# Optimization experiments

Hardware: AMD Instinct MI355X
Metric: run time of the kernel (lower is better)

## Reference

```python
import jax, jax.numpy as jnp
import numpy as np

NR = 5000            # number of sampled center points
H, W = 480, 640      # depth map resolution
P = NR * (NR - 1) // 2  # number of ordered pairs (i < j) = 12,497,500


def setup_inputs() -> dict:
    key = jax.random.key(0)
    k1, k2, k3, k4 = jax.random.split(key, 4)
    x = jax.random.normal(k1, (H, W), dtype=jnp.float32)
    rows = jax.random.randint(k2, (NR,), 0, H)
    cols = jax.random.randint(k3, (NR,), 0, W)
    centers = jnp.stack([rows, cols], axis=1).astype(jnp.int32)  # [NR, 2]
    # relative-depth ground truth labels in {-1, 0, +1}; mask = |gt|
    gt = jax.random.randint(k4, (P,), -1, 2).astype(jnp.float32)
    return {"x": x, "gt": gt, "centers": centers}


def reference(x, gt, centers):
    # gather predicted depths at the NR sampled pixel locations
    z = x[centers[:, 0], centers[:, 1]]            # [NR]
    # all pairs i<j in the same row-major order as the original double loop
    ii, jj = jnp.triu_indices(NR, k=1)             # each [P]
    d = z[ii] - z[jj]                              # z_A - z_B, [P]
    mask = jnp.abs(gt)                             # [P]
    # logistic ranking loss where gt != 0, squared loss where gt == 0
    loss = mask * jnp.log1p(jnp.exp(-gt * d)) + (1.0 - mask) * d * d
    return jnp.sum(loss) / jnp.float32(P)
```

## Files before the change

kernel.cpp:

```cpp
#include <hip/hip_runtime.h>
#include <stdint.h>

#define NR 5000
#define NRM1 4999
#define W 640
#define NBLK 2500
#define NG 5
#define PCOUNT 12497500.0f
#define LOG2E 1.44269504088896340736f
#define LN2   0.69314718055994530942f

typedef float float4u __attribute__((ext_vector_type(4)));
struct __attribute__((packed, aligned(4))) f4wrap { float4u v; };

__device__ __forceinline__ float4u load4u(const float* p) {
    return ((const f4wrap*)p)->v;
}

__global__ void gather_z(const float* __restrict__ x,
                         const int* __restrict__ centers,
                         float* __restrict__ z) {
    int t = blockIdx.x * blockDim.x + threadIdx.x;
    if (t < NR) {
        const int2 rc = ((const int2*)centers)[t];
        z[t] = x[rc.x * W + rc.y];
    }
}

__global__ __launch_bounds__(256) void pair_loss(const float* __restrict__ gt,
                                                 const float* __restrict__ z,
                                                 float* __restrict__ partials) {
    __shared__ float sz[NR];
    __shared__ float wsum[4];
    const int tid = threadIdx.x;
    const int b = blockIdx.x;

    const float4* __restrict__ zf4 = (const float4*)z;
    for (int t = tid; t < NR / 4; t += 256)
        *(float4*)&sz[4 * t] = zf4[t];
    __syncthreads();

    const int r1 = b, r2 = NR - 2 - b;
    const int len1 = NRM1 - r1;
    const int off1 = r1 * NRM1 - (r1 * (r1 - 1)) / 2;
    const int off2 = r2 * NRM1 - (r2 * (r2 - 1)) / 2;
    const int off2v = off2 - len1;
    const int vmax = (r2 > r1) ? 5000 : len1;
    const float zr1 = sz[r1], zr2 = sz[r2];

    float4u g4[NG];
    int cb[NG];
    #pragma unroll
    for (int k = 0; k < NG; ++k) {
        const int vb = 4 * tid + 1024 * k;
        const int c = min(vb, vmax - 4);
        cb[k] = c;
        const float* base = (c < len1) ? (gt + off1) : (gt + off2v);
        g4[k] = load4u(base + c);
    }
    #pragma unroll
    for (int k = 0; k < NG; ++k) {
        const int c = cb[k];
        if (c < len1 && c + 3 >= len1) {
            #pragma unroll
            for (int e = 0; e < 4; ++e)
                if (c + e >= len1) g4[k][e] = gt[off2v + c + e];
        }
    }

    float a0 = 0.0f, a1 = 0.0f, a2 = 0.0f, a3 = 0.0f;
    #pragma unroll
    for (int k = 0; k < NG; ++k) {
        const int c = cb[k];
        float l[4];
        #pragma unroll
        for (int e = 0; e < 4; ++e) {
            const int ce = c + e;
            const bool in1 = ce < len1;
            const float zj = sz[ce + (in1 ? r1 + 1 : 0)];
            const float zr = in1 ? zr1 : zr2;
            const float g = g4[k][e];
            const float s  = zj - zr;
            const float sl = s * LOG2E;
            const float lg = __log2f(1.0f + exp2f(g * sl));
            l[e] = (g != 0.0f) ? lg : s * sl;
        }
        const float gs = (l[0] + l[1]) + (l[2] + l[3]);
        const float gv = (4 * tid + 1024 * k < vmax) ? gs : 0.0f;
        if      ((k & 3) == 0) a0 += gv;
        else if ((k & 3) == 1) a1 += gv;
        else if ((k & 3) == 2) a2 += gv;
        else                   a3 += gv;
    }
    float acc = (a0 + a1) + (a2 + a3);

    for (int o = 32; o > 0; o >>= 1) acc += __shfl_down(acc, o, 64);
    if ((tid & 63) == 0) wsum[tid >> 6] = acc;
    __syncthreads();
    if (tid == 0)
        partials[b] = (wsum[0] + wsum[1]) + (wsum[2] + wsum[3]);
}

__global__ __launch_bounds__(256) void final_reduce(const float* __restrict__ partials,
                                                    float* __restrict__ out) {
    __shared__ float wsum[4];
    float acc = 0.0f;
    const float4* __restrict__ p4 = (const float4*)partials;
    for (int t = threadIdx.x; t < NBLK / 4; t += 256) {
        const float4 v = p4[t];
        acc += (v.x + v.y) + (v.z + v.w);
    }
    for (int o = 32; o > 0; o >>= 1) acc += __shfl_down(acc, o, 64);
    if ((threadIdx.x & 63) == 0) wsum[threadIdx.x >> 6] = acc;
    __syncthreads();
    if (threadIdx.x == 0)
        out[0] = ((wsum[0] + wsum[1]) + (wsum[2] + wsum[3])) * (LN2 / PCOUNT);
}

extern "C" void kernel_launch(void* const* d_in, const int* in_sizes, int n_in,
                              void* d_out, int out_size, void* d_ws, size_t ws_size,
                              hipStream_t stream) {
    const float* x       = (const float*)d_in[0];
    const float* gt      = (const float*)d_in[1];
    const int*   centers = (const int*)d_in[2];
    float* out = (float*)d_out;

    float* z        = (float*)d_ws;
    float* partials = z + NR;

    gather_z<<<(NR + 255) / 256, 256, 0, stream>>>(x, centers, z);
    pair_loss<<<NBLK, 256, 0, stream>>>(gt, z, partials);
    final_reduce<<<1, 256, 0, stream>>>(partials, out);
}
```

Before: 25.22 us.

## Compute pairwise loss in packed fp16 with pre-scaled, shifted half2 z arrays

Stores the gathered depths as pre-scaled (by log2e) fp16 pairs in two arrays offset by one element, so each thread can read eight z values with one aligned 16-byte load regardless of row parity. This removes the shared-memory staging and its barrier. The loss is evaluated branch-free with packed half2 math: softplus via exp2/log2, plus a squared term weighted by (1-g^2). Each thread handles 8 pairs per group instead of 4, and partial sums are accumulated in half2. fp16 accumulation and transcendental evaluation cut ALU work but risk significant precision loss, and adding ~5000 terms per block in half may overflow the tolerance.

```diff
diff --git a/kernel.cpp b/kernel.cpp
--- a/kernel.cpp
+++ b/kernel.cpp
@@ -1,98 +1,132 @@
 #include <hip/hip_runtime.h>
+#include <hip/hip_fp16.h>
 #include <stdint.h>
 
 #define NR 5000
 #define NRM1 4999
 #define W 640
 #define NBLK 2500
-#define NG 5
+#define PTOT 12497500
 #define PCOUNT 12497500.0f
 #define LOG2E 1.44269504088896340736f
 #define LN2   0.69314718055994530942f
+#define NH2   2512
 
 typedef float float4u __attribute__((ext_vector_type(4)));
 struct __attribute__((packed, aligned(4))) f4wrap { float4u v; };
-
 __device__ __forceinline__ float4u load4u(const float* p) {
     return ((const f4wrap*)p)->v;
+}
+__device__ __forceinline__ __half2 f2h2(float f) {
+    union { float f; __half2 h; } u; u.f = f; return u.h;
 }
 
 __global__ void gather_z(const float* __restrict__ x,
                          const int* __restrict__ centers,
-                         float* __restrict__ z) {
-    int t = blockIdx.x * blockDim.x + threadIdx.x;
-    if (t < NR) {
-        const int2 rc = ((const int2*)centers)[t];
-        z[t] = x[rc.x * W + rc.y];
+                         __half2* __restrict__ zsA,
+                         __half2* __restrict__ zsB) {
+    const int i = blockIdx.x * blockDim.x + threadIdx.x;
+    if (i >= NH2) return;
+    float v[3];
+    #pragma unroll
+    for (int e = 0; e < 3; ++e) {
+        const int t = 2 * i + e;
+        if (t < NR) {
+            const int2 rc = ((const int2*)centers)[t];
+            v[e] = x[rc.x * W + rc.y] * LOG2E;
+        } else {
+            v[e] = 0.0f;
+        }
     }
+    zsA[i] = __floats2half2_rn(v[0], v[1]);
+    zsB[i] = __floats2half2_rn(v[1], v[2]);
 }
 
 __global__ __launch_bounds__(256) void pair_loss(const float* __restrict__ gt,
-                                                 const float* __restrict__ z,
+                                                 const __half2* __restrict__ zsA,
+                                                 const __half2* __restrict__ zsB,
                                                  float* __restrict__ partials) {
-    __shared__ float sz[NR];
     __shared__ float wsum[4];
     const int tid = threadIdx.x;
     const int b = blockIdx.x;
 
-    const float4* __restrict__ zf4 = (const float4*)z;
-    for (int t = tid; t < NR / 4; t += 256)
-        *(float4*)&sz[4 * t] = zf4[t];
-    __syncthreads();
-
     const int r1 = b, r2 = NR - 2 - b;
-    const int len1 = NRM1 - r1;
+    const int len1 = NRM1 - b;
+    const int len1p = (len1 + 7) & ~7;
+    const int len2 = (r2 > r1) ? (b + 1) : 0;
+    const int vmaxp = len1p + len2;
     const int off1 = r1 * NRM1 - (r1 * (r1 - 1)) / 2;
     const int off2 = r2 * NRM1 - (r2 * (r2 - 1)) / 2;
-    const int off2v = off2 - len1;
-    const int vmax = (r2 > r1) ? 5000 : len1;
-    const float zr1 = sz[r1], zr2 = sz[r2];
+    const int off2p = off2 - len1p;
+    const int j1 = r1 + 1;
+    const int j2 = r2 + 1 - len1p;
+    const __half2* __restrict__ pz1 = (j1 & 1) ? zsB : zsA;
+    const __half2* __restrict__ pz2 = (j2 & 1) ? zsB : zsA;
+    const int h1 = j1 >> 1;
+    const int h2o = j2 >> 1;
+    const int G = (vmaxp - 1) & ~7;
 
-    float4u g4[NG];
-    int cb[NG];
-    #pragma unroll
-    for (int k = 0; k < NG; ++k) {
-        const int vb = 4 * tid + 1024 * k;
-        const int c = min(vb, vmax - 4);
-        cb[k] = c;
-        const float* base = (c < len1) ? (gt + off1) : (gt + off2v);
-        g4[k] = load4u(base + c);
-    }
-    #pragma unroll
-    for (int k = 0; k < NG; ++k) {
-        const int c = cb[k];
-        if (c < len1 && c + 3 >= len1) {
-            #pragma unroll
-            for (int e = 0; e < 4; ++e)
-                if (c + e >= len1) g4[k][e] = gt[off2v + c + e];
+    const __half* __restrict__ zflat = (const __half*)zsA;
+    const __half2 zr1h = __half2half2(zflat[r1]);
+    const __half2 zr2h = __half2half2(zflat[r2]);
+    const __half2 one2 = __float2half2_rn(1.0f);
+    const __half2 ln2h = __float2half2_rn(LN2);
+    const __half2 neg1 = __float2half2_rn(-1.0f);
+
+    __half2 acc01 = __float2half2_rn(0.0f);
+    __half2 acc23 = __float2half2_rn(0.0f);
+    float accS = 0.0f;
+
+    auto doGroup = [&](int vb) {
+        const int c = min(vb, G);
+        const bool isr2 = c >= len1p;
+        int gidx = (isr2 ? off2p : off1) + c;
+        gidx = min(gidx, PTOT - 8);
+        const float4u ga = load4u(gt + gidx);
+        const float4u gb = load4u(gt + gidx + 4);
+        const __half2* zb = isr2 ? pz2 : pz1;
+        const int zi = (c >> 1) + (isr2 ? h2o : h1);
+        const float4u zraw = load4u((const float*)zb + zi);
+        const __half2 zr = isr2 ? zr2h : zr1h;
+        const __half2 zj[4] = { f2h2(zraw.x), f2h2(zraw.y), f2h2(zraw.z), f2h2(zraw.w) };
+        const __half2 gh[4] = { __floats2half2_rn(ga.x, ga.y), __floats2half2_rn(ga.z, ga.w),
+                                __floats2half2_rn(gb.x, gb.y), __floats2half2_rn(gb.z, gb.w) };
+        __half2 l[4];
+        #pragma unroll
+        for (int m = 0; m < 4; ++m) {
+            const __half2 s  = __hsub2(zj[m], zr);
+            const __half2 t  = __hmul2(gh[m], s);
+            const __half2 lg = h2log2(__hadd2(h2exp2(t), one2));
+            const __half2 q1 = __hfma2(__hmul2(s, ln2h), s, neg1);
+            const __half2 wm = __hfma2(__hneg2(gh[m]), gh[m], one2);
+            l[m] = __hfma2(wm, q1, lg);
         }
-    }
+        const int lim = isr2 ? vmaxp : len1;
+        if (vb == c) {
+            if (c + 8 <= lim) {
+                acc01 = __hadd2(acc01, __hadd2(l[0], l[1]));
+                acc23 = __hadd2(acc23, __hadd2(l[2], l[3]));
+            } else {
+                float fs = 0.0f;
+                #pragma unroll
+                for (int m = 0; m < 4; ++m) {
+                    const float2 lf = __half22float2(l[m]);
+                    if (c + 2 * m     < lim) fs += lf.x;
+                    if (c + 2 * m + 1 < lim) fs += lf.y;
+                }
+                accS += fs;
+            }
+        }
+    };
 
-    float a0 = 0.0f, a1 = 0.0f, a2 = 0.0f, a3 = 0.0f;
-    #pragma unroll
-    for (int k = 0; k < NG; ++k) {
-        const int c = cb[k];
-        float l[4];
-        #pragma unroll
-        for (int e = 0; e < 4; ++e) {
-            const int ce = c + e;
-            const bool in1 = ce < len1;
-            const float zj = sz[ce + (in1 ? r1 + 1 : 0)];
-            const float zr = in1 ? zr1 : zr2;
-            const float g = g4[k][e];
-            const float s  = zj - zr;
-            const float sl = s * LOG2E;
-            const float lg = __log2f(1.0f + exp2f(g * sl));
-            l[e] = (g != 0.0f) ? lg : s * sl;
-        }
-        const float gs = (l[0] + l[1]) + (l[2] + l[3]);
-        const float gv = (4 * tid + 1024 * k < vmax) ? gs : 0.0f;
-        if      ((k & 3) == 0) a0 += gv;
-        else if ((k & 3) == 1) a1 += gv;
-        else if ((k & 3) == 2) a2 += gv;
-        else                   a3 += gv;
-    }
-    float acc = (a0 + a1) + (a2 + a3);
+    doGroup(8 * tid);
+    doGroup(8 * tid + 2048);
+    const int vb2 = 8 * tid + 4096;
+    if (vb2 <= G) doGroup(vb2);
+
+    const float2 f01 = __half22float2(acc01);
+    const float2 f23 = __half22float2(acc23);
+    float acc = ((f01.x + f01.y) + (f23.x + f23.y)) + accS;
 
     for (int o = 32; o > 0; o >>= 1) acc += __shfl_down(acc, o, 64);
     if ((tid & 63) == 0) wsum[tid >> 6] = acc;
@@ -125,10 +159,11 @@
     const int*   centers = (const int*)d_in[2];
     float* out = (float*)d_out;
 
-    float* z        = (float*)d_ws;
-    float* partials = z + NR;
+    __half2* zsA   = (__half2*)d_ws;
+    __half2* zsB   = zsA + NH2;
+    float* partials = (float*)(zsB + NH2);
 
-    gather_z<<<(NR + 255) / 256, 256, 0, stream>>>(x, centers, z);
-    pair_loss<<<NBLK, 256, 0, stream>>>(gt, z, partials);
+    gather_z<<<(NH2 + 255) / 256, 256, 0, stream>>>(x, centers, zsA, zsB);
+    pair_loss<<<NBLK, 256, 0, stream>>>(gt, zsA, zsB, partials);
     final_reduce<<<1, 256, 0, stream>>>(partials, out);
 }
```

Measured after the change: 22.29 us. -11.6%, faster.
